# Performance work log

Hardware: AMD Instinct MI355X
Metric: run time of the kernel (lower is better)

The kernel has to match this reference:

```python
import jax, jax.numpy as jnp
import numpy as np

BITS = 4
MAXQ = (1 << BITS) - 1          # 15
PACK = 32 // BITS               # 8 values per int32
GROUP = 128
CLIPMIN = 1e-5
CLIPMAX = 1e4


def _unpack_rows(qweight, infeatures):
    # qweight: [in/PACK, out] int32; values packed along the row (infeatures) dim.
    shifts = (jnp.arange(PACK, dtype=jnp.int32) * BITS)[None, :, None]   # [1,PACK,1]
    w = (qweight[:, None, :] >> shifts) & MAXQ                            # [in/PACK, PACK, out]
    return w.reshape(-1, qweight.shape[1])[:infeatures].astype(jnp.float32)


def setup_inputs() -> dict:
    key = jax.random.key(0)
    k1, k2, k3, k4, k5 = jax.random.split(key, 5)
    infeatures, outfeatures, tokens = 4096, 4096, 2048
    num_groups = infeatures // GROUP
    x = jax.random.normal(k1, (tokens, infeatures), dtype=jnp.float32)
    # positive scales, well inside [CLIPMIN, CLIPMAX]
    scales = jax.random.uniform(k2, (num_groups, outfeatures), dtype=jnp.float32,
                                minval=0.005, maxval=0.02)
    # zero points roughly centered in the quant range [0, 15]
    zero_points = jax.random.uniform(k3, (num_groups, outfeatures), dtype=jnp.float32,
                                     minval=0.0, maxval=float(MAXQ))
    bias = jax.random.normal(k4, (outfeatures,), dtype=jnp.float32)
    qweight = jax.random.randint(k5, (infeatures // PACK, outfeatures),
                                 jnp.iinfo(jnp.int32).min, jnp.iinfo(jnp.int32).max,
                                 dtype=jnp.int32)
    return {"x": x, "scales": scales, "zero_points": zero_points,
            "bias": bias, "qweight": qweight}


def reference(x, scales, zero_points, bias, qweight):
    infeatures = x.shape[-1]
    out_f = scales.shape[1]
    num_groups = scales.shape[0]
    w = _unpack_rows(qweight, infeatures)                       # [in, out] fp32 in [0,15]
    s = jnp.clip(scales, CLIPMIN, CLIPMAX)                      # [G, out]
    z = jnp.clip(jnp.round(zero_points), 0.0, float(MAXQ))      # [G, out]
    wg = w.reshape(num_groups, GROUP, out_f)                    # [G, group, out]
    deq = ((wg - z[:, None, :]) * s[:, None, :]).reshape(infeatures, out_f)
    return x @ deq + bias
```

## Files before the change

kernel.cpp:

```cpp
#include <hip/hip_runtime.h>
#include <cstdint>
#include <cstddef>

typedef __attribute__((ext_vector_type(8))) short short8;
typedef __attribute__((ext_vector_type(4))) float floatx4;

typedef __attribute__((address_space(1))) const void gvoid_t;
typedef __attribute__((address_space(3))) void lvoid_t;

__device__ inline short f2bf(float f) {
    unsigned u = __float_as_uint(f);
    u = (u + 0x7FFFu + ((u >> 16) & 1u)) >> 16;
    return (short)u;
}

__global__ __launch_bounds__(256) void prologue_kernel(
    const float* __restrict__ x, short* __restrict__ xb, long long nx, int ncvt,
    const int* __restrict__ qw, const float* __restrict__ scales,
    const float* __restrict__ zps, short* __restrict__ deqT,
    int N, int K, int nbx)
{
    __shared__ int lds_q[32 * 65];
    const int t = threadIdx.x;

    if ((int)blockIdx.x < ncvt) {
        long long i = ((long long)blockIdx.x * 256 + t) * 8;
        if (i + 8 > nx) return;
        const float4* p = (const float4*)(x + i);
        float4 v0 = p[0];
        float4 v1 = p[1];
        short8 h;
        h[0] = f2bf(v0.x); h[1] = f2bf(v0.y); h[2] = f2bf(v0.z); h[3] = f2bf(v0.w);
        h[4] = f2bf(v1.x); h[5] = f2bf(v1.y); h[6] = f2bf(v1.z); h[7] = f2bf(v1.w);
        *(short8*)(xb + i) = h;
        return;
    }

    const int b2 = (int)blockIdx.x - ncvt;
    const int n0 = (b2 % nbx) * 64;
    const int r0 = (b2 / nbx) * 32;

    #pragma unroll
    for (int v = 0; v < 2; ++v) {
        int idx = t + v * 256;
        int row = idx >> 4;
        int c4  = (idx & 15) * 4;
        const int4 q4 = *(const int4*)(qw + (size_t)(r0 + row) * N + n0 + c4);
        int base = row * 65 + c4;
        lds_q[base + 0] = q4.x;
        lds_q[base + 1] = q4.y;
        lds_q[base + 2] = q4.z;
        lds_q[base + 3] = q4.w;
    }
    __syncthreads();

    const int L  = t & 63;
    const int w  = t >> 6;
    const int rq = L & 31;
    const int hi = L >> 5;
    const int g  = (r0 + rq) >> 4;

    #pragma unroll
    for (int it = 0; it < 8; ++it) {
        const int p  = w * 8 + it;
        const int nl = 2 * p + hi;

        float s = scales[(size_t)g * N + n0 + nl];
        s = fminf(fmaxf(s, 1e-5f), 1e4f);
        float z = rintf(zps[(size_t)g * N + n0 + nl]);
        z = fminf(fmaxf(z, 0.0f), 15.0f);

        const int q = lds_q[rq * 65 + nl];
        short8 h;
        #pragma unroll
        for (int j = 0; j < 8; ++j) {
            float f = (float)((q >> (4 * j)) & 15);
            h[j] = f2bf((f - z) * s);
        }
        *(short8*)(deqT + (size_t)(n0 + nl) * K + (size_t)(r0 + rq) * 8) = h;
    }
}

#define BM 128
#define BN 256
#define BK 64

#define LGKM0_FENCE() do { \
    asm volatile("s_waitcnt lgkmcnt(0)" ::: "memory"); \
    __builtin_amdgcn_sched_barrier(0); \
} while (0)

__global__ __launch_bounds__(512, 2) void gemm_bf16_bt(
    const short* __restrict__ A, const short* __restrict__ Bt,
    const float* __restrict__ bias, float* __restrict__ C,
    int M, int N, int K)
{
    __shared__ __align__(16) short a_lds[2][BM * BK];
    __shared__ __align__(16) short b_lds[2][BN * BK];

    const int t = threadIdx.x;
    const int L = t & 63;
    const int w = t >> 6;

    const int nbn = N / BN;
    const int id  = blockIdx.x;
    int nt, mt;
    if ((nbn & 7) == 0) {
        const int xcd = id & 7;
        const int loc = id >> 3;
        const int gsz = nbn >> 3;
        nt = xcd * gsz + (loc % gsz);
        mt = loc / gsz;
    } else {
        nt = id % nbn;
        mt = id / nbn;
    }
    const int m0 = mt * BM;
    const int n0 = nt * BN;

    const int wm = (w & 1) * 64;
    const int wn = (w >> 1) * 64;

    floatx4 acc[4][4] = {};

    const int sr = L >> 3;
    const int sc = L & 7;
    const int gc = sc ^ sr;
    const short* ag = A  + (size_t)(m0 + w * 8 + sr) * K + gc * 8;
    const short* bg = Bt + (size_t)(n0 + w * 8 + sr) * K + gc * 8;
    const int adst = (w * 8) * BK;

    const int NT = K / BK;

    const int l15 = L & 15, l4 = L >> 4, l7 = L & 7;
    const int p0 = l4 ^ l7;
    const int p1 = (4 + l4) ^ l7;

#define STAGE(kt_, buf_) do { \
    const size_t ko_ = (size_t)(kt_) * BK; \
    __builtin_amdgcn_global_load_lds((gvoid_t*)(ag + ko_), \
        (lvoid_t*)(&a_lds[buf_][adst]), 16, 0, 0); \
    __builtin_amdgcn_global_load_lds((gvoid_t*)(ag + (size_t)64 * K + ko_), \
        (lvoid_t*)(&a_lds[buf_][adst + 64 * BK]), 16, 0, 0); \
    __builtin_amdgcn_global_load_lds((gvoid_t*)(bg + ko_), \
        (lvoid_t*)(&b_lds[buf_][adst]), 16, 0, 0); \
    __builtin_amdgcn_global_load_lds((gvoid_t*)(bg + (size_t)64 * K + ko_), \
        (lvoid_t*)(&b_lds[buf_][adst + 64 * BK]), 16, 0, 0); \
    __builtin_amdgcn_global_load_lds((gvoid_t*)(bg + (size_t)128 * K + ko_), \
        (lvoid_t*)(&b_lds[buf_][adst + 128 * BK]), 16, 0, 0); \
    __builtin_amdgcn_global_load_lds((gvoid_t*)(bg + (size_t)192 * K + ko_), \
        (lvoid_t*)(&b_lds[buf_][adst + 192 * BK]), 16, 0, 0); \
} while (0)

    STAGE(0, 0);
    STAGE(1, 1);
    asm volatile("s_waitcnt vmcnt(6)" ::: "memory");
    __builtin_amdgcn_s_barrier();

    for (int ti = 0; ti < NT; ++ti) {
        const int cur = ti & 1;
        short8 a0[4], a1[4], b0f[4], b1f[4];

        #pragma unroll
        for (int i = 0; i < 4; ++i)
            a0[i] = *(const short8*)(&a_lds[cur][(wm + 16 * i + l15) * BK + p0 * 8]);
        #pragma unroll
        for (int j = 0; j < 2; ++j)
            b0f[j] = *(const short8*)(&b_lds[cur][(wn + 16 * j + l15) * BK + p0 * 8]);
        LGKM0_FENCE();
        __builtin_amdgcn_s_barrier();
        __builtin_amdgcn_s_setprio(1);
        #pragma unroll
        for (int i = 0; i < 4; ++i) {
            acc[i][0] = __builtin_amdgcn_mfma_f32_16x16x32_bf16(a0[i], b0f[0], acc[i][0], 0, 0, 0);
            acc[i][1] = __builtin_amdgcn_mfma_f32_16x16x32_bf16(a0[i], b0f[1], acc[i][1], 0, 0, 0);
        }
        __builtin_amdgcn_s_setprio(0);
        __builtin_amdgcn_s_barrier();

        #pragma unroll
        for (int j = 2; j < 4; ++j)
            b0f[j] = *(const short8*)(&b_lds[cur][(wn + 16 * j + l15) * BK + p0 * 8]);
        LGKM0_FENCE();
        __builtin_amdgcn_s_barrier();
        __builtin_amdgcn_s_setprio(1);
        #pragma unroll
        for (int i = 0; i < 4; ++i) {
            acc[i][2] = __builtin_amdgcn_mfma_f32_16x16x32_bf16(a0[i], b0f[2], acc[i][2], 0, 0, 0);
            acc[i][3] = __builtin_amdgcn_mfma_f32_16x16x32_bf16(a0[i], b0f[3], acc[i][3], 0, 0, 0);
        }
        __builtin_amdgcn_s_setprio(0);
        __builtin_amdgcn_s_barrier();

        #pragma unroll
        for (int i = 0; i < 4; ++i)
            a1[i] = *(const short8*)(&a_lds[cur][(wm + 16 * i + l15) * BK + p1 * 8]);
        #pragma unroll
        for (int j = 0; j < 2; ++j)
            b1f[j] = *(const short8*)(&b_lds[cur][(wn + 16 * j + l15) * BK + p1 * 8]);
        LGKM0_FENCE();
        __builtin_amdgcn_s_barrier();
        __builtin_amdgcn_s_setprio(1);
        #pragma unroll
        for (int i = 0; i < 4; ++i) {
            acc[i][0] = __builtin_amdgcn_mfma_f32_16x16x32_bf16(a1[i], b1f[0], acc[i][0], 0, 0, 0);
            acc[i][1] = __builtin_amdgcn_mfma_f32_16x16x32_bf16(a1[i], b1f[1], acc[i][1], 0, 0, 0);
        }
        __builtin_amdgcn_s_setprio(0);
        __builtin_amdgcn_s_barrier();

        #pragma unroll
        for (int j = 2; j < 4; ++j)
            b1f[j] = *(const short8*)(&b_lds[cur][(wn + 16 * j + l15) * BK + p1 * 8]);
        LGKM0_FENCE();
        __builtin_amdgcn_s_barrier();
        if (ti + 2 < NT) {
            STAGE(ti + 2, cur);
        }
        __builtin_amdgcn_s_setprio(1);
        #pragma unroll
        for (int i = 0; i < 4; ++i) {
            acc[i][2] = __builtin_amdgcn_mfma_f32_16x16x32_bf16(a1[i], b1f[2], acc[i][2], 0, 0, 0);
            acc[i][3] = __builtin_amdgcn_mfma_f32_16x16x32_bf16(a1[i], b1f[3], acc[i][3], 0, 0, 0);
        }
        __builtin_amdgcn_s_setprio(0);
        if (ti + 2 < NT) {
            asm volatile("s_waitcnt vmcnt(6)" ::: "memory");
        } else if (ti + 1 < NT) {
            asm volatile("s_waitcnt vmcnt(0)" ::: "memory");
        }
        __builtin_amdgcn_s_barrier();
    }

    float bv[4];
    #pragma unroll
    for (int j = 0; j < 4; ++j)
        bv[j] = bias[n0 + wn + 16 * j + l15];
    const int col0 = n0 + wn + l15;
    #pragma unroll
    for (int i = 0; i < 4; ++i) {
        const int row0 = m0 + wm + 16 * i + l4 * 4;
        #pragma unroll
        for (int r = 0; r < 4; ++r) {
            float* outr = C + (size_t)(row0 + r) * N + col0;
            #pragma unroll
            for (int j = 0; j < 4; ++j)
                outr[16 * j] = acc[i][j][r] + bv[j];
        }
    }
}

extern "C" void kernel_launch(void* const* d_in, const int* in_sizes, int n_in,
                              void* d_out, int out_size, void* d_ws, size_t ws_size,
                              hipStream_t stream)
{
    const float* x      = (const float*)d_in[0];
    const float* scales = (const float*)d_in[1];
    const float* zps    = (const float*)d_in[2];
    const float* bias   = (const float*)d_in[3];
    const int*   qw     = (const int*)d_in[4];

    const int N = in_sizes[3];
    const int G = in_sizes[1] / N;
    const int K = G * 128;
    const int M = in_sizes[0] / K;

    short* xb   = (short*)d_ws;
    short* deqT = xb + (size_t)M * K;
    float* out  = (float*)d_out;

    const long long nx = (long long)M * K;
    const int ncvt = (int)(nx / 2048);
    const int nbx  = N / 64;
    const int ndq  = nbx * (K / 256);

    prologue_kernel<<<ncvt + ndq, 256, 0, stream>>>(
        x, xb, nx, ncvt, qw, scales, zps, deqT, N, K, nbx);
    gemm_bf16_bt<<<dim3((M / BM) * (N / BN)), 512, 0, stream>>>(
        xb, deqT, bias, out, M, N, K);
}
```

Measured before the change: 198.7 us.

## Triple-buffer LDS tiles and issue next-stage loads at iteration start

```diff
diff --git a/kernel.cpp b/kernel.cpp
--- a/kernel.cpp
+++ b/kernel.cpp
@@ -84,6 +84,7 @@
 #define BM 128
 #define BN 256
 #define BK 64
+#define NBUF 3
 
 #define LGKM0_FENCE() do { \
     asm volatile("s_waitcnt lgkmcnt(0)" ::: "memory"); \
@@ -95,8 +96,8 @@
     const float* __restrict__ bias, float* __restrict__ C,
     int M, int N, int K)
 {
-    __shared__ __align__(16) short a_lds[2][BM * BK];
-    __shared__ __align__(16) short b_lds[2][BN * BK];
+    __shared__ __align__(16) short a_lds[NBUF][BM * BK];
+    __shared__ __align__(16) short b_lds[NBUF][BN * BK];
 
     const int t = threadIdx.x;
     const int L = t & 63;
@@ -157,71 +158,50 @@
     asm volatile("s_waitcnt vmcnt(6)" ::: "memory");
     __builtin_amdgcn_s_barrier();
 
+    int cur = 0;
     for (int ti = 0; ti < NT; ++ti) {
-        const int cur = ti & 1;
+        const int prv = (cur == 0) ? 2 : cur - 1;
+        const short* ab = &a_lds[cur][0];
+        const short* bb = &b_lds[cur][0];
         short8 a0[4], a1[4], b0f[4], b1f[4];
 
         #pragma unroll
         for (int i = 0; i < 4; ++i)
-            a0[i] = *(const short8*)(&a_lds[cur][(wm + 16 * i + l15) * BK + p0 * 8]);
-        #pragma unroll
-        for (int j = 0; j < 2; ++j)
-            b0f[j] = *(const short8*)(&b_lds[cur][(wn + 16 * j + l15) * BK + p0 * 8]);
+            a0[i] = *(const short8*)(ab + (wm + 16 * i + l15) * BK + p0 * 8);
+        #pragma unroll
+        for (int j = 0; j < 4; ++j)
+            b0f[j] = *(const short8*)(bb + (wn + 16 * j + l15) * BK + p0 * 8);
+        if (ti + 2 < NT) {
+            STAGE(ti + 2, prv);
+        }
+        __builtin_amdgcn_s_barrier();
         LGKM0_FENCE();
-        __builtin_amdgcn_s_barrier();
         __builtin_amdgcn_s_setprio(1);
         #pragma unroll
         for (int i = 0; i < 4; ++i) {
-            acc[i][0] = __builtin_amdgcn_mfma_f32_16x16x32_bf16(a0[i], b0f[0], acc[i][0], 0, 0, 0);
-            acc[i][1] = __builtin_amdgcn_mfma_f32_16x16x32_bf16(a0[i], b0f[1], acc[i][1], 0, 0, 0);
+            #pragma unroll
+            for (int j = 0; j < 4; ++j)
+                acc[i][j] = __builtin_amdgcn_mfma_f32_16x16x32_bf16(
+                    a0[i], b0f[j], acc[i][j], 0, 0, 0);
         }
         __builtin_amdgcn_s_setprio(0);
         __builtin_amdgcn_s_barrier();
 
         #pragma unroll
-        for (int j = 2; j < 4; ++j)
-            b0f[j] = *(const short8*)(&b_lds[cur][(wn + 16 * j + l15) * BK + p0 * 8]);
+        for (int i = 0; i < 4; ++i)
+            a1[i] = *(const short8*)(ab + (wm + 16 * i + l15) * BK + p1 * 8);
+        #pragma unroll
+        for (int j = 0; j < 4; ++j)
+            b1f[j] = *(const short8*)(bb + (wn + 16 * j + l15) * BK + p1 * 8);
+        __builtin_amdgcn_s_barrier();
         LGKM0_FENCE();
-        __builtin_amdgcn_s_barrier();
         __builtin_amdgcn_s_setprio(1);
         #pragma unroll
         for (int i = 0; i < 4; ++i) {
-            acc[i][2] = __builtin_amdgcn_mfma_f32_16x16x32_bf16(a0[i], b0f[2], acc[i][2], 0, 0, 0);
-            acc[i][3] = __builtin_amdgcn_mfma_f32_16x16x32_bf16(a0[i], b0f[3], acc[i][3], 0, 0, 0);
-        }
-        __builtin_amdgcn_s_setprio(0);
-        __builtin_amdgcn_s_barrier();
-
-        #pragma unroll
-        for (int i = 0; i < 4; ++i)
-            a1[i] = *(const short8*)(&a_lds[cur][(wm + 16 * i + l15) * BK + p1 * 8]);
-        #pragma unroll
-        for (int j = 0; j < 2; ++j)
-            b1f[j] = *(const short8*)(&b_lds[cur][(wn + 16 * j + l15) * BK + p1 * 8]);
-        LGKM0_FENCE();
-        __builtin_amdgcn_s_barrier();
-        __builtin_amdgcn_s_setprio(1);
-        #pragma unroll
-        for (int i = 0; i < 4; ++i) {
-            acc[i][0] = __builtin_amdgcn_mfma_f32_16x16x32_bf16(a1[i], b1f[0], acc[i][0], 0, 0, 0);
-            acc[i][1] = __builtin_amdgcn_mfma_f32_16x16x32_bf16(a1[i], b1f[1], acc[i][1], 0, 0, 0);
-        }
-        __builtin_amdgcn_s_setprio(0);
-        __builtin_amdgcn_s_barrier();
-
-        #pragma unroll
-        for (int j = 2; j < 4; ++j)
-            b1f[j] = *(const short8*)(&b_lds[cur][(wn + 16 * j + l15) * BK + p1 * 8]);
-        LGKM0_FENCE();
-        __builtin_amdgcn_s_barrier();
-        if (ti + 2 < NT) {
-            STAGE(ti + 2, cur);
-        }
-        __builtin_amdgcn_s_setprio(1);
-        #pragma unroll
-        for (int i = 0; i < 4; ++i) {
-            acc[i][2] = __builtin_amdgcn_mfma_f32_16x16x32_bf16(a1[i], b1f[2], acc[i][2], 0, 0, 0);
-            acc[i][3] = __builtin_amdgcn_mfma_f32_16x16x32_bf16(a1[i], b1f[3], acc[i][3], 0, 0, 0);
+            #pragma unroll
+            for (int j = 0; j < 4; ++j)
+                acc[i][j] = __builtin_amdgcn_mfma_f32_16x16x32_bf16(
+                    a1[i], b1f[j], acc[i][j], 0, 0, 0);
         }
         __builtin_amdgcn_s_setprio(0);
         if (ti + 2 < NT) {
@@ -230,6 +210,8 @@
             asm volatile("s_waitcnt vmcnt(0)" ::: "memory");
         }
         __builtin_amdgcn_s_barrier();
+
+        cur = (cur == 2) ? 0 : cur + 1;
     }
 
     float bv[4];
```

Result: faster. 180.2 us (-9.3%).
